# Performance work log

Hardware: AMD Instinct MI355X
Metric: run time of the kernel (lower is better)

The kernel has to match this reference:

```python
import jax, jax.numpy as jnp
import numpy as np

N = 100000   # nodes
E = 1600000  # edges
D = 64       # hidden dim == num_features
L = 3        # num_gc_layers
C = 10       # num_classes
G = 512      # num graphs in batch
BN_EPS = 1e-5


def setup_inputs() -> dict:
    key = jax.random.key(0)
    ks = jax.random.split(key, 12)
    s = 1.0 / np.sqrt(D)
    return {
        "x": jax.random.normal(ks[0], (N, D), dtype=jnp.float32),
        "edge_index": jax.random.randint(ks[1], (2, E), 0, N, dtype=jnp.int64),
        "batch": jnp.sort(jax.random.randint(ks[2], (N,), 0, G, dtype=jnp.int64)),
        # GINConv MLP params (layer 0 input dim == D, so all layers stack)
        "w1": jax.random.normal(ks[3], (L, D, D), dtype=jnp.float32) * s,
        "b1": jnp.zeros((L, D), dtype=jnp.float32),
        "w2": jax.random.normal(ks[4], (L, D, D), dtype=jnp.float32) * s,
        "b2": jnp.zeros((L, D), dtype=jnp.float32),
        # BatchNorm affine params
        "gamma": jnp.ones((L, D), dtype=jnp.float32),
        "beta": jnp.zeros((L, D), dtype=jnp.float32),
        # final MLP
        "lin_w": jax.random.normal(ks[5], (L * D, D), dtype=jnp.float32) / np.sqrt(L * D),
        "lin_b": jnp.zeros((D,), dtype=jnp.float32),
        "fin_w": jax.random.normal(ks[6], (D, C), dtype=jnp.float32) * s,
        "fin_b": jnp.zeros((C,), dtype=jnp.float32),
    }


def reference(x, edge_index, batch, w1, b1, w2, b2, gamma, beta, lin_w, lin_b, fin_w, fin_b):
    src, dst = edge_index[0], edge_index[1]
    pooled = []
    h = x
    for i in range(L):
        # GINConv (eps=0): (1+eps)*h_i + sum_{j->i} h_j, then 2-layer MLP
        agg = h + jax.ops.segment_sum(h[src], dst, num_segments=N)  # [N, D]
        z = jax.nn.relu(agg @ w1[i] + b1[i]) @ w2[i] + b2[i]
        z = jax.nn.relu(z)
        # BatchNorm1d (training-mode batch statistics, biased variance)
        mean = jnp.mean(z, axis=0)
        var = jnp.var(z, axis=0)
        h = (z - mean) * (gamma[i] / jnp.sqrt(var + BN_EPS)) + beta[i]
        # global_add_pool: segment-sum over graph ids
        pooled.append(jax.ops.segment_sum(h, batch, num_segments=G))  # [G, D]
    xp = jnp.concatenate(pooled, axis=1)  # [G, L*D]
    out = jax.nn.relu(xp @ lin_w + lin_b) @ fin_w + fin_b  # [G, C]
    return jax.nn.log_softmax(out, axis=-1)
```

## Files before the change

### kernel.cpp

```cpp
#include <hip/hip_runtime.h>

#define BN_EPS 1e-5f
#define TN 128
#define NPB 256
#define BCAP 8192
#define BH_EPB 8192
#define PT_EPB 4096

typedef __attribute__((ext_vector_type(8))) short bf16x8;
typedef __attribute__((ext_vector_type(4))) float f32x4;

static __device__ __forceinline__ unsigned short f2bf(float f) {
    unsigned u = __float_as_uint(f);
    u += 0x7fff + ((u >> 16) & 1);
    return (unsigned short)(u >> 16);
}
static __device__ __forceinline__ float bf2f(unsigned short s) {
    return __uint_as_float(((unsigned)s) << 16);
}

__global__ __launch_bounds__(256) void xbf_kernel(
    const float* __restrict__ x, unsigned short* __restrict__ xbf, int n4)
{
    const int i = blockIdx.x * 256 + threadIdx.x;
    if (i < n4) {
        const float4 v = reinterpret_cast<const float4*>(x)[i];
        ushort4 o;
        o.x = f2bf(v.x); o.y = f2bf(v.y); o.z = f2bf(v.z); o.w = f2bf(v.w);
        reinterpret_cast<ushort4*>(xbf)[i] = o;
    }
}

__global__ __launch_bounds__(256) void wtbf_kernel(
    const float* __restrict__ w1, const float* __restrict__ w2,
    unsigned short* __restrict__ wtb)
{
    __shared__ float sT[64 * 65];
    const int b = blockIdx.x;
    const int t = threadIdx.x;
    const float* src = ((b & 1) ? w2 : w1) + (size_t)(b >> 1) * 4096;
#pragma unroll
    for (int rr = 0; rr < 4; ++rr) {
        const int i = (rr * 256 + t) * 4;
        const float4 v = *reinterpret_cast<const float4*>(src + i);
        const int k = i >> 6, j = i & 63;
        sT[(j + 0) * 65 + k] = v.x;
        sT[(j + 1) * 65 + k] = v.y;
        sT[(j + 2) * 65 + k] = v.z;
        sT[(j + 3) * 65 + k] = v.w;
    }
    __syncthreads();
    const int j = t >> 2;
    const int kb = (t & 3) * 16;
    unsigned short o[16];
#pragma unroll
    for (int i = 0; i < 16; ++i) o[i] = f2bf(sT[j * 65 + kb + i]);
    uint4* dp = reinterpret_cast<uint4*>(wtb + ((size_t)b * 64 + j) * 64 + kb);
    dp[0] = *reinterpret_cast<const uint4*>(&o[0]);
    dp[1] = *reinterpret_cast<const uint4*>(&o[8]);
}

__global__ __launch_bounds__(256) void bh_kernel(
    const int* __restrict__ dst, int* __restrict__ bucketCnt, int E, int NB)
{
    __shared__ int lh[512];
    const int tid = threadIdx.x;
    for (int i = tid; i < NB; i += 256) lh[i] = 0;
    __syncthreads();
    const int base = blockIdx.x * BH_EPB;
#pragma unroll
    for (int k = 0; k < BH_EPB / 256; ++k) {
        const int e = base + k * 256 + tid;
        if (e < E) atomicAdd(&lh[dst[e] >> 8], 1);
    }
    __syncthreads();
    for (int i = tid; i < NB; i += 256) {
        const int c = lh[i];
        if (c > 0) atomicAdd(&bucketCnt[i], c);
    }
}

__global__ __launch_bounds__(512) void bscan_kernel(
    const int* __restrict__ bucketCnt, int* __restrict__ bucketStart,
    int* __restrict__ bucketCursor, int NB)
{
    __shared__ int ls[512];
    const int t = threadIdx.x;
    const int v = (t < NB) ? bucketCnt[t] : 0;
    ls[t] = v;
    __syncthreads();
    for (int off = 1; off < 512; off <<= 1) {
        const int a = ls[t];
        const int b = (t >= off) ? ls[t - off] : 0;
        __syncthreads();
        ls[t] = a + b;
        __syncthreads();
    }
    const int excl = ls[t] - v;
    if (t < NB) { bucketStart[t] = excl; bucketCursor[t] = excl; }
    if (t == 511) bucketStart[NB] = ls[511];
}

__global__ __launch_bounds__(256) void part_kernel(
    const int* __restrict__ src, const int* __restrict__ dst,
    int* __restrict__ bucketCursor, unsigned* __restrict__ part, int E, int NB)
{
    __shared__ int lh[512];
    __shared__ int lbase[512];
    const int tid = threadIdx.x;
    const int base = blockIdx.x * PT_EPB;
    for (int i = tid; i < NB; i += 256) lh[i] = 0;
    __syncthreads();
#pragma unroll
    for (int k = 0; k < PT_EPB / 256; ++k) {
        const int e = base + k * 256 + tid;
        if (e < E) atomicAdd(&lh[dst[e] >> 8], 1);
    }
    __syncthreads();
    for (int i = tid; i < NB; i += 256) {
        const int c = lh[i];
        lbase[i] = (c > 0) ? atomicAdd(&bucketCursor[i], c) : 0;
        lh[i] = 0;
    }
    __syncthreads();
#pragma unroll
    for (int k = 0; k < PT_EPB / 256; ++k) {
        const int e = base + k * 256 + tid;
        if (e < E) {
            const int d = dst[e];
            const int b = d >> 8;
            const int off = atomicAdd(&lh[b], 1);
            part[lbase[b] + off] = ((unsigned)src[e] << 8) | (unsigned)(d & 255);
        }
    }
}

__global__ __launch_bounds__(256) void bcsr_kernel(
    const unsigned* __restrict__ part, const int* __restrict__ bucketStart,
    int* __restrict__ deg, int* __restrict__ rowstart,
    int* __restrict__ eidx, int nN)
{
    __shared__ unsigned sSrc[BCAP];
    __shared__ int ldeg[256], ls[256], lcur[256];
    const int b = blockIdx.x;
    const int tid = threadIdx.x;
    const int sStart = bucketStart[b];
    const int cnt = bucketStart[b + 1] - sStart;
    const bool ldsok = (cnt <= BCAP);

    ldeg[tid] = 0;
    __syncthreads();
    for (int i = tid; i < cnt; i += 256) {
        const unsigned v = part[sStart + i];
        if (ldsok) sSrc[i] = v;
        atomicAdd(&ldeg[v & 255u], 1);
    }
    __syncthreads();
    const int dv = ldeg[tid];
    ls[tid] = dv;
    __syncthreads();
    for (int off = 1; off < 256; off <<= 1) {
        const int a = ls[tid];
        const int c = (tid >= off) ? ls[tid - off] : 0;
        __syncthreads();
        ls[tid] = a + c;
        __syncthreads();
    }
    const int excl = ls[tid] - dv;
    lcur[tid] = excl;
    const int node = b * NPB + tid;
    if (node < nN) {
        deg[node] = dv;
        rowstart[node] = sStart + excl;
    }
    __syncthreads();
    for (int i = tid; i < cnt; i += 256) {
        const unsigned v = ldsok ? sSrc[i] : part[sStart + i];
        const int dloc = (int)(v & 255u);
        const int p = atomicAdd(&lcur[dloc], 1);
        eidx[sStart + p] = (int)(v >> 8);
    }
}

__global__ __launch_bounds__(256) void cnt_kernel(
    const int* __restrict__ batch, int* __restrict__ cnt, int nN)
{
    const int n = blockIdx.x * 256 + threadIdx.x;
    if (n >= nN) return;
    const int g = batch[n];
    const bool firstb = (n == 0) || (batch[n - 1] != g);
    const bool lastb  = (n == nN - 1) || (batch[n + 1] != g);
    if (lastb)  atomicAdd(&cnt[g], n + 1);
    if (firstb) atomicAdd(&cnt[g], -n);
}

__global__ __launch_bounds__(256) void agg_kernel(
    const unsigned short* __restrict__ z, const float* __restrict__ scsh,
    const int* __restrict__ rowstart, const int* __restrict__ deg,
    const int* __restrict__ eidx, unsigned short* __restrict__ agg, int nN)
{
    const int node = blockIdx.x * 4 + (threadIdx.x >> 6);
    if (node >= nN) return;
    const int lane = threadIdx.x & 63;
    const int q = lane >> 4;
    const int fr = (lane & 15) * 4;
    const int rs = rowstart[node];
    const int d = deg[node];

    float a0 = 0.f, a1 = 0.f, a2 = 0.f, a3 = 0.f;
    if (q == 0) {
        const ushort4 v = *reinterpret_cast<const ushort4*>(z + (size_t)node * 64 + fr);
        a0 = bf2f(v.x); a1 = bf2f(v.y); a2 = bf2f(v.z); a3 = bf2f(v.w);
    }
    for (int i = 0; i < d; i += 16) {
        const int j0 = i + q, j1 = j0 + 4, j2 = j0 + 8, j3 = j0 + 12;
        const int c0 = min(j0, d - 1), c1 = min(j1, d - 1);
        const int c2 = min(j2, d - 1), c3 = min(j3, d - 1);
        const int s0 = eidx[rs + c0], s1 = eidx[rs + c1];
        const int s2 = eidx[rs + c2], s3 = eidx[rs + c3];
        const ushort4 v0 = *reinterpret_cast<const ushort4*>(z + (size_t)s0 * 64 + fr);
        const ushort4 v1 = *reinterpret_cast<const ushort4*>(z + (size_t)s1 * 64 + fr);
        const ushort4 v2 = *reinterpret_cast<const ushort4*>(z + (size_t)s2 * 64 + fr);
        const ushort4 v3 = *reinterpret_cast<const ushort4*>(z + (size_t)s3 * 64 + fr);
        const float w0 = (j0 < d) ? 1.f : 0.f;
        const float w1 = (j1 < d) ? 1.f : 0.f;
        const float w2 = (j2 < d) ? 1.f : 0.f;
        const float w3 = (j3 < d) ? 1.f : 0.f;
        a0 = fmaf(w0, bf2f(v0.x), a0); a1 = fmaf(w0, bf2f(v0.y), a1);
        a2 = fmaf(w0, bf2f(v0.z), a2); a3 = fmaf(w0, bf2f(v0.w), a3);
        a0 = fmaf(w1, bf2f(v1.x), a0); a1 = fmaf(w1, bf2f(v1.y), a1);
        a2 = fmaf(w1, bf2f(v1.z), a2); a3 = fmaf(w1, bf2f(v1.w), a3);
        a0 = fmaf(w2, bf2f(v2.x), a0); a1 = fmaf(w2, bf2f(v2.y), a1);
        a2 = fmaf(w2, bf2f(v2.z), a2); a3 = fmaf(w2, bf2f(v2.w), a3);
        a0 = fmaf(w3, bf2f(v3.x), a0); a1 = fmaf(w3, bf2f(v3.y), a1);
        a2 = fmaf(w3, bf2f(v3.z), a2); a3 = fmaf(w3, bf2f(v3.w), a3);
    }
    a0 += __shfl_xor(a0, 16); a0 += __shfl_xor(a0, 32);
    a1 += __shfl_xor(a1, 16); a1 += __shfl_xor(a1, 32);
    a2 += __shfl_xor(a2, 16); a2 += __shfl_xor(a2, 32);
    a3 += __shfl_xor(a3, 16); a3 += __shfl_xor(a3, 32);
    if (lane < 16) {
        float4 sc = make_float4(1.f, 1.f, 1.f, 1.f);
        float4 sh = make_float4(0.f, 0.f, 0.f, 0.f);
        if (scsh) {
            sc = *reinterpret_cast<const float4*>(scsh + fr);
            sh = *reinterpret_cast<const float4*>(scsh + 64 + fr);
        }
        const float c = (float)(d + 1);
        ushort4 ob;
        ob.x = f2bf(fmaf(a0, sc.x, c * sh.x));
        ob.y = f2bf(fmaf(a1, sc.y, c * sh.y));
        ob.z = f2bf(fmaf(a2, sc.z, c * sh.z));
        ob.w = f2bf(fmaf(a3, sc.w, c * sh.w));
        *reinterpret_cast<ushort4*>(agg + (size_t)node * 64 + fr) = ob;
    }
}

__global__ __launch_bounds__(256) void mlp_kernel(
    const unsigned short* __restrict__ agg, const int* __restrict__ batch,
    const unsigned short* __restrict__ wtb, const float* __restrict__ b1,
    const float* __restrict__ b2,
    unsigned short* __restrict__ zout, float* __restrict__ bnstats,
    float* __restrict__ xpz, int layer, int nN, int storeZ)
{
    __shared__ unsigned short sA[128 * 72];
    __shared__ unsigned short sW[2][64 * 72];
    __shared__ float sB[2][64];
    __shared__ float sSum[64], sSq[64];
    __shared__ float sPool[4 * 64];
    __shared__ int sBatch[128];

    const int tid = threadIdx.x;
    const int n0 = blockIdx.x * TN;

    {
        const int row = tid >> 1;
        const int cg = (tid & 1) * 32;
        const int node = n0 + row;
        uint4 v0 = make_uint4(0, 0, 0, 0), v1 = v0, v2 = v0, v3 = v0;
        if (node < nN) {
            const uint4* g = reinterpret_cast<const uint4*>(agg + (size_t)node * 64 + cg);
            v0 = g[0]; v1 = g[1]; v2 = g[2]; v3 = g[3];
        }
        uint4* dp = reinterpret_cast<uint4*>(&sA[row * 72 + cg]);
        dp[0] = v0; dp[1] = v1; dp[2] = v2; dp[3] = v3;
    }
    {
        const int m = tid >> 7;
        const int j = (tid & 127) >> 1;
        const int cg = (tid & 1) * 32;
        const uint4* g = reinterpret_cast<const uint4*>(
            wtb + (((size_t)layer * 2 + m) * 64 + j) * 64 + cg);
        uint4* dp = reinterpret_cast<uint4*>(&sW[m][j * 72 + cg]);
        dp[0] = g[0]; dp[1] = g[1]; dp[2] = g[2]; dp[3] = g[3];
        if (tid < 64) {
            sB[0][tid] = b1[layer * 64 + tid];
            sB[1][tid] = b2[layer * 64 + tid];
            sSum[tid] = 0.f; sSq[tid] = 0.f;
        }
        if (tid < 128) sBatch[tid] = (n0 + tid < nN) ? batch[n0 + tid] : -1;
        sPool[tid] = 0.f;
    }
    __syncthreads();

    const int w  = tid >> 6;
    const int l  = tid & 63;
    const int lr = l & 15;
    const int hi = l >> 4;

    f32x4 acc[2][4];
#pragma unroll
    for (int rt = 0; rt < 2; ++rt)
#pragma unroll
        for (int ct = 0; ct < 4; ++ct) {
            const float bv = sB[0][ct * 16 + lr];
            acc[rt][ct] = (f32x4){bv, bv, bv, bv};
        }
#pragma unroll
    for (int kb = 0; kb < 2; ++kb) {
        const bf16x8 af0 = *reinterpret_cast<const bf16x8*>(&sA[(w * 32 + lr) * 72 + kb * 32 + hi * 8]);
        const bf16x8 af1 = *reinterpret_cast<const bf16x8*>(&sA[(w * 32 + 16 + lr) * 72 + kb * 32 + hi * 8]);
#pragma unroll
        for (int ct = 0; ct < 4; ++ct) {
            const bf16x8 bfr = *reinterpret_cast<const bf16x8*>(&sW[0][(ct * 16 + lr) * 72 + kb * 32 + hi * 8]);
            acc[0][ct] = __builtin_amdgcn_mfma_f32_16x16x32_bf16(af0, bfr, acc[0][ct], 0, 0, 0);
            acc[1][ct] = __builtin_amdgcn_mfma_f32_16x16x32_bf16(af1, bfr, acc[1][ct], 0, 0, 0);
        }
    }
    __syncthreads();
#pragma unroll
    for (int rt = 0; rt < 2; ++rt)
#pragma unroll
        for (int ct = 0; ct < 4; ++ct)
#pragma unroll
            for (int r = 0; r < 4; ++r)
                sA[(w * 32 + rt * 16 + hi * 4 + r) * 72 + ct * 16 + lr] =
                    f2bf(fmaxf(acc[rt][ct][r], 0.f));
    __syncthreads();

#pragma unroll
    for (int rt = 0; rt < 2; ++rt)
#pragma unroll
        for (int ct = 0; ct < 4; ++ct) {
            const float bv = sB[1][ct * 16 + lr];
            acc[rt][ct] = (f32x4){bv, bv, bv, bv};
        }
#pragma unroll
    for (int kb = 0; kb < 2; ++kb) {
        const bf16x8 af0 = *reinterpret_cast<const bf16x8*>(&sA[(w * 32 + lr) * 72 + kb * 32 + hi * 8]);
        const bf16x8 af1 = *reinterpret_cast<const bf16x8*>(&sA[(w * 32 + 16 + lr) * 72 + kb * 32 + hi * 8]);
#pragma unroll
        for (int ct = 0; ct < 4; ++ct) {
            const bf16x8 bfr = *reinterpret_cast<const bf16x8*>(&sW[1][(ct * 16 + lr) * 72 + kb * 32 + hi * 8]);
            acc[0][ct] = __builtin_amdgcn_mfma_f32_16x16x32_bf16(af0, bfr, acc[0][ct], 0, 0, 0);
            acc[1][ct] = __builtin_amdgcn_mfma_f32_16x16x32_bf16(af1, bfr, acc[1][ct], 0, 0, 0);
        }
    }

    const int gfirst = sBatch[0];
#pragma unroll
    for (int ct = 0; ct < 4; ++ct) {
        const int j = ct * 16 + lr;
        float s = 0.f, qsum = 0.f;
#pragma unroll
        for (int rt = 0; rt < 2; ++rt) {
            int curg = -1;
            float ps = 0.f;
#pragma unroll
            for (int r = 0; r < 4; ++r) {
                const int lrow = w * 32 + rt * 16 + hi * 4 + r;
                const int node = n0 + lrow;
                const float v = fmaxf(acc[rt][ct][r], 0.f);
                if (node < nN) {
                    if (storeZ) zout[(size_t)node * 64 + j] = f2bf(v);
                    s += v; qsum += v * v;
                    const int g = sBatch[lrow];
                    if (g != curg) {
                        if (curg >= 0) {
                            const int lg = curg - gfirst;
                            if (lg < 4) atomicAdd(&sPool[lg * 64 + j], ps);
                            else        atomicAdd(&xpz[(size_t)curg * 64 + j], ps);
                        }
                        curg = g; ps = 0.f;
                    }
                    ps += v;
                }
            }
            if (curg >= 0) {
                const int lg = curg - gfirst;
                if (lg < 4) atomicAdd(&sPool[lg * 64 + j], ps);
                else        atomicAdd(&xpz[(size_t)curg * 64 + j], ps);
            }
        }
        s += __shfl_xor(s, 16); s += __shfl_xor(s, 32);
        qsum += __shfl_xor(qsum, 16); qsum += __shfl_xor(qsum, 32);
        if (hi == 0) { atomicAdd(&sSum[j], s); atomicAdd(&sSq[j], qsum); }
    }
    __syncthreads();
    {
        const int lg = tid >> 6, d = tid & 63;
        const float v = sPool[tid];
        if (v != 0.f) atomicAdd(&xpz[(size_t)(gfirst + lg) * 64 + d], v);
    }
    if (tid < 64) {
        atomicAdd(&bnstats[tid], sSum[tid]);
        atomicAdd(&bnstats[64 + tid], sSq[tid]);
    }
}

__global__ __launch_bounds__(256) void finalize_kernel(
    float* __restrict__ xp, const float* __restrict__ bnstats,
    const float* __restrict__ gamma, const float* __restrict__ beta,
    const int* __restrict__ cnt, float* __restrict__ xpz,
    float* __restrict__ scsh, int layer, int nG, float invN)
{
    const int i = blockIdx.x * 256 + threadIdx.x;
    if (i >= nG * 64) return;
    const int g = i >> 6, d = i & 63;
    const float mean = bnstats[d] * invN;
    const float var  = fmaxf(bnstats[64 + d] * invN - mean * mean, 0.f);
    const float sc = gamma[layer * 64 + d] * rsqrtf(var + BN_EPS);
    const float sh = beta[layer * 64 + d] - mean * sc;
    if (g == 0) { scsh[d] = sc; scsh[64 + d] = sh; }
    xp[(size_t)g * 192 + layer * 64 + d] = fmaf(sc, xpz[i], (float)cnt[g] * sh);
    xpz[i] = 0.f;
}

__global__ __launch_bounds__(256) void final_kernel(
    const float* __restrict__ xp, const float* __restrict__ lin_w,
    const float* __restrict__ lin_b, const float* __restrict__ fin_w,
    const float* __restrict__ fin_b, float* __restrict__ out, int nG)
{
    const int g = (blockIdx.x * 256 + threadIdx.x) >> 6;
    const int lane = threadIdx.x & 63;
    if (g >= nG) return;
    const float* xr = xp + (size_t)g * 192;
    float acc = lin_b[lane];
    for (int k = 0; k < 192; ++k) acc = fmaf(xr[k], lin_w[k * 64 + lane], acc);
    const float t = fmaxf(acc, 0.f);
    float o[10];
#pragma unroll
    for (int c = 0; c < 10; ++c) {
        float p = t * fin_w[lane * 10 + c];
#pragma unroll
        for (int off = 32; off > 0; off >>= 1) p += __shfl_xor(p, off);
        o[c] = p + fin_b[c];
    }
    float m = o[0];
#pragma unroll
    for (int c = 1; c < 10; ++c) m = fmaxf(m, o[c]);
    float Z = 0.f;
#pragma unroll
    for (int c = 0; c < 10; ++c) Z += expf(o[c] - m);
    const float lz = m + logf(Z);
#pragma unroll
    for (int c = 0; c < 10; ++c)
        if (lane == c) out[(size_t)g * 10 + c] = o[c] - lz;
}

extern "C" void kernel_launch(void* const* d_in, const int* in_sizes, int n_in,
                              void* d_out, int out_size, void* d_ws, size_t ws_size,
                              hipStream_t stream)
{
    const float* x     = (const float*)d_in[0];
    const int*   ei    = (const int*)d_in[1];
    const int*   batch = (const int*)d_in[2];
    const float* w1    = (const float*)d_in[3];
    const float* b1    = (const float*)d_in[4];
    const float* w2    = (const float*)d_in[5];
    const float* b2    = (const float*)d_in[6];
    const float* gamma = (const float*)d_in[7];
    const float* beta  = (const float*)d_in[8];
    const float* lin_w = (const float*)d_in[9];
    const float* lin_b = (const float*)d_in[10];
    const float* fin_w = (const float*)d_in[11];
    const float* fin_b = (const float*)d_in[12];
    float* out = (float*)d_out;

    const int N = in_sizes[0] / 64;
    const int E = in_sizes[1] / 2;
    const int L = in_sizes[3] / 4096;
    const int G = out_size / 10;
    const float invN = 1.0f / (float)N;
    const int NB = (N + NPB - 1) / NPB;

    char* ws = (char*)d_ws;
    size_t off = 0;
    auto alloc = [&](size_t bytes) -> void* {
        void* p = ws + off;
        off += (bytes + 255) & ~(size_t)255;
        return p;
    };
    unsigned short* xbf = (unsigned short*)alloc((size_t)N * 64 * 2);
    unsigned short* z0  = (unsigned short*)alloc((size_t)N * 64 * 2);
    unsigned short* z1  = (unsigned short*)alloc((size_t)N * 64 * 2);
    unsigned short* aggbuf = (unsigned short*)alloc((size_t)N * 64 * 2);
    unsigned short* wtb = (unsigned short*)alloc((size_t)L * 2 * 4096 * 2);
    float* xp      = (float*)alloc((size_t)G * 192 * 4);
    float* xpz     = (float*)alloc((size_t)G * 64 * 4);
    float* bnstats = (float*)alloc((size_t)L * 128 * 4);
    float* scsh    = (float*)alloc(128 * 4);
    int*   cnt      = (int*)alloc((size_t)G * 4);
    int*   deg      = (int*)alloc((size_t)N * 4);
    int*   rowstart = (int*)alloc((size_t)N * 4);
    int*   eidx     = (int*)alloc((size_t)E * 4);
    unsigned* part  = (unsigned*)alloc((size_t)E * 4);
    int*   bucketCnt    = (int*)alloc((size_t)NB * 4);
    int*   bucketStart  = (int*)alloc((size_t)(NB + 1) * 4);
    int*   bucketCursor = (int*)alloc((size_t)NB * 4);

    const int* srcIdx = ei;
    const int* dstIdx = ei + E;

    hipMemsetAsync(bucketCnt, 0, (size_t)NB * 4, stream);
    hipMemsetAsync(bnstats, 0, (size_t)L * 128 * 4, stream);
    hipMemsetAsync(xpz, 0, (size_t)G * 64 * 4, stream);
    hipMemsetAsync(cnt, 0, (size_t)G * 4, stream);
    bh_kernel<<<(E + BH_EPB - 1) / BH_EPB, 256, 0, stream>>>(dstIdx, bucketCnt, E, NB);
    bscan_kernel<<<1, 512, 0, stream>>>(bucketCnt, bucketStart, bucketCursor, NB);
    part_kernel<<<(E + PT_EPB - 1) / PT_EPB, 256, 0, stream>>>(
        srcIdx, dstIdx, bucketCursor, part, E, NB);
    bcsr_kernel<<<NB, 256, 0, stream>>>(part, bucketStart, deg, rowstart, eidx, N);
    cnt_kernel<<<(N + 255) / 256, 256, 0, stream>>>(batch, cnt, N);
    xbf_kernel<<<(N * 16 + 255) / 256, 256, 0, stream>>>(x, xbf, N * 16);
    wtbf_kernel<<<L * 2, 256, 0, stream>>>(w1, w2, wtb);

    const int nAggBlk = (N + 3) / 4;
    const int nMlpBlk = (N + TN - 1) / TN;
    unsigned short* zprev = xbf;
    unsigned short* zcur = z0;
    for (int l = 0; l < L; ++l) {
        agg_kernel<<<nAggBlk, 256, 0, stream>>>(
            zprev, (l == 0) ? nullptr : scsh,
            rowstart, deg, eidx, aggbuf, N);
        mlp_kernel<<<nMlpBlk, 256, 0, stream>>>(
            aggbuf, batch, wtb, b1, b2,
            zcur, bnstats + (size_t)l * 128, xpz, l, N, (l < L - 1) ? 1 : 0);
        finalize_kernel<<<(G * 64 + 255) / 256, 256, 0, stream>>>(
            xp, bnstats + (size_t)l * 128, gamma, beta, cnt, xpz, scsh, l, G, invN);
        zprev = zcur;
        zcur = (zcur == z0) ? z1 : z0;
    }
    final_kernel<<<(G * 64 + 255) / 256, 256, 0, stream>>>(xp, lin_w, lin_b,
                                                           fin_w, fin_b, out, G);
}
```

Before: 323.3 us.

## Fold BN finalize into agg and head kernels, merge prep launches and memsets

Removes the per-layer finalize kernel: the BN scale and shift are recomputed from the raw stats inside agg_kernel, and the pooled outputs of every layer are kept in separate per-layer buffers that a single head kernel normalizes before the final MLP. The xbf, cnt and weight-transpose kernels are merged into one prep launch, and the four memsets become one contiguous memset. The goal is to cut kernel launches and the serial dependencies between them, at the price of redundant per-thread BN math in agg_kernel and a larger pooled buffer.

```diff
diff --git a/kernel.cpp b/kernel.cpp
--- a/kernel.cpp
+++ b/kernel.cpp
@@ -19,26 +19,38 @@
     return __uint_as_float(((unsigned)s) << 16);
 }
 
-__global__ __launch_bounds__(256) void xbf_kernel(
-    const float* __restrict__ x, unsigned short* __restrict__ xbf, int n4)
-{
-    const int i = blockIdx.x * 256 + threadIdx.x;
-    if (i < n4) {
-        const float4 v = reinterpret_cast<const float4*>(x)[i];
-        ushort4 o;
-        o.x = f2bf(v.x); o.y = f2bf(v.y); o.z = f2bf(v.z); o.w = f2bf(v.w);
-        reinterpret_cast<ushort4*>(xbf)[i] = o;
-    }
-}
-
-__global__ __launch_bounds__(256) void wtbf_kernel(
+__global__ __launch_bounds__(256) void prep_kernel(
+    const float* __restrict__ x, unsigned short* __restrict__ xbf, int n4, int n4b,
+    const int* __restrict__ batch, int* __restrict__ cnt, int nN, int ncb,
     const float* __restrict__ w1, const float* __restrict__ w2,
     unsigned short* __restrict__ wtb)
 {
     __shared__ float sT[64 * 65];
     const int b = blockIdx.x;
     const int t = threadIdx.x;
-    const float* src = ((b & 1) ? w2 : w1) + (size_t)(b >> 1) * 4096;
+    if (b < n4b) {
+        const int i = b * 256 + t;
+        if (i < n4) {
+            const float4 v = reinterpret_cast<const float4*>(x)[i];
+            ushort4 o;
+            o.x = f2bf(v.x); o.y = f2bf(v.y); o.z = f2bf(v.z); o.w = f2bf(v.w);
+            reinterpret_cast<ushort4*>(xbf)[i] = o;
+        }
+        return;
+    }
+    if (b < n4b + ncb) {
+        const int n = (b - n4b) * 256 + t;
+        if (n < nN) {
+            const int g = batch[n];
+            const bool firstb = (n == 0) || (batch[n - 1] != g);
+            const bool lastb  = (n == nN - 1) || (batch[n + 1] != g);
+            if (lastb)  atomicAdd(&cnt[g], n + 1);
+            if (firstb) atomicAdd(&cnt[g], -n);
+        }
+        return;
+    }
+    const int bw = b - n4b - ncb;
+    const float* src = ((bw & 1) ? w2 : w1) + (size_t)(bw >> 1) * 4096;
 #pragma unroll
     for (int rr = 0; rr < 4; ++rr) {
         const int i = (rr * 256 + t) * 4;
@@ -55,7 +67,7 @@
     unsigned short o[16];
 #pragma unroll
     for (int i = 0; i < 16; ++i) o[i] = f2bf(sT[j * 65 + kb + i]);
-    uint4* dp = reinterpret_cast<uint4*>(wtb + ((size_t)b * 64 + j) * 64 + kb);
+    uint4* dp = reinterpret_cast<uint4*>(wtb + ((size_t)bw * 64 + j) * 64 + kb);
     dp[0] = *reinterpret_cast<const uint4*>(&o[0]);
     dp[1] = *reinterpret_cast<const uint4*>(&o[8]);
 }
@@ -182,22 +194,12 @@
     }
 }
 
-__global__ __launch_bounds__(256) void cnt_kernel(
-    const int* __restrict__ batch, int* __restrict__ cnt, int nN)
-{
-    const int n = blockIdx.x * 256 + threadIdx.x;
-    if (n >= nN) return;
-    const int g = batch[n];
-    const bool firstb = (n == 0) || (batch[n - 1] != g);
-    const bool lastb  = (n == nN - 1) || (batch[n + 1] != g);
-    if (lastb)  atomicAdd(&cnt[g], n + 1);
-    if (firstb) atomicAdd(&cnt[g], -n);
-}
-
 __global__ __launch_bounds__(256) void agg_kernel(
-    const unsigned short* __restrict__ z, const float* __restrict__ scsh,
+    const unsigned short* __restrict__ z, const float* __restrict__ bnprev,
+    const float* __restrict__ gamma, const float* __restrict__ beta,
     const int* __restrict__ rowstart, const int* __restrict__ deg,
-    const int* __restrict__ eidx, unsigned short* __restrict__ agg, int nN)
+    const int* __restrict__ eidx, unsigned short* __restrict__ agg,
+    int layerPrev, int nN, float invN)
 {
     const int node = blockIdx.x * 4 + (threadIdx.x >> 6);
     if (node >= nN) return;
@@ -240,18 +242,23 @@
     a2 += __shfl_xor(a2, 16); a2 += __shfl_xor(a2, 32);
     a3 += __shfl_xor(a3, 16); a3 += __shfl_xor(a3, 32);
     if (lane < 16) {
-        float4 sc = make_float4(1.f, 1.f, 1.f, 1.f);
-        float4 sh = make_float4(0.f, 0.f, 0.f, 0.f);
-        if (scsh) {
-            sc = *reinterpret_cast<const float4*>(scsh + fr);
-            sh = *reinterpret_cast<const float4*>(scsh + 64 + fr);
+        float sc[4] = {1.f, 1.f, 1.f, 1.f};
+        float sh[4] = {0.f, 0.f, 0.f, 0.f};
+        if (bnprev) {
+#pragma unroll
+            for (int k = 0; k < 4; ++k) {
+                const float mean = bnprev[fr + k] * invN;
+                const float var = fmaxf(bnprev[64 + fr + k] * invN - mean * mean, 0.f);
+                sc[k] = gamma[layerPrev * 64 + fr + k] * rsqrtf(var + BN_EPS);
+                sh[k] = beta[layerPrev * 64 + fr + k] - mean * sc[k];
+            }
         }
         const float c = (float)(d + 1);
         ushort4 ob;
-        ob.x = f2bf(fmaf(a0, sc.x, c * sh.x));
-        ob.y = f2bf(fmaf(a1, sc.y, c * sh.y));
-        ob.z = f2bf(fmaf(a2, sc.z, c * sh.z));
-        ob.w = f2bf(fmaf(a3, sc.w, c * sh.w));
+        ob.x = f2bf(fmaf(a0, sc[0], c * sh[0]));
+        ob.y = f2bf(fmaf(a1, sc[1], c * sh[1]));
+        ob.z = f2bf(fmaf(a2, sc[2], c * sh[2]));
+        ob.w = f2bf(fmaf(a3, sc[3], c * sh[3]));
         *reinterpret_cast<ushort4*>(agg + (size_t)node * 64 + fr) = ob;
     }
 }
@@ -408,34 +415,33 @@
     }
 }
 
-__global__ __launch_bounds__(256) void finalize_kernel(
-    float* __restrict__ xp, const float* __restrict__ bnstats,
+__global__ __launch_bounds__(256) void head_kernel(
+    const float* __restrict__ xpz, const float* __restrict__ bnstats,
     const float* __restrict__ gamma, const float* __restrict__ beta,
-    const int* __restrict__ cnt, float* __restrict__ xpz,
-    float* __restrict__ scsh, int layer, int nG, float invN)
-{
-    const int i = blockIdx.x * 256 + threadIdx.x;
-    if (i >= nG * 64) return;
-    const int g = i >> 6, d = i & 63;
-    const float mean = bnstats[d] * invN;
-    const float var  = fmaxf(bnstats[64 + d] * invN - mean * mean, 0.f);
-    const float sc = gamma[layer * 64 + d] * rsqrtf(var + BN_EPS);
-    const float sh = beta[layer * 64 + d] - mean * sc;
-    if (g == 0) { scsh[d] = sc; scsh[64 + d] = sh; }
-    xp[(size_t)g * 192 + layer * 64 + d] = fmaf(sc, xpz[i], (float)cnt[g] * sh);
-    xpz[i] = 0.f;
-}
-
-__global__ __launch_bounds__(256) void final_kernel(
-    const float* __restrict__ xp, const float* __restrict__ lin_w,
-    const float* __restrict__ lin_b, const float* __restrict__ fin_w,
-    const float* __restrict__ fin_b, float* __restrict__ out, int nG)
-{
-    const int g = (blockIdx.x * 256 + threadIdx.x) >> 6;
+    const int* __restrict__ cnt,
+    const float* __restrict__ lin_w, const float* __restrict__ lin_b,
+    const float* __restrict__ fin_w, const float* __restrict__ fin_b,
+    float* __restrict__ out, int nG, int nL, float invN)
+{
+    __shared__ float sX[4][192];
+    const int wv = threadIdx.x >> 6;
     const int lane = threadIdx.x & 63;
-    if (g >= nG) return;
-    const float* xr = xp + (size_t)g * 192;
+    const int g = blockIdx.x * 4 + wv;
+    const bool act = (g < nG);
+    const float cg = act ? (float)cnt[g] : 0.f;
+    const size_t G64 = (size_t)nG * 64;
+    for (int ll = 0; ll < nL; ++ll) {
+        const float mean = bnstats[ll * 128 + lane] * invN;
+        const float var  = fmaxf(bnstats[ll * 128 + 64 + lane] * invN - mean * mean, 0.f);
+        const float sc = gamma[ll * 64 + lane] * rsqrtf(var + BN_EPS);
+        const float sh = beta[ll * 64 + lane] - mean * sc;
+        const float pv = act ? xpz[ll * G64 + (size_t)g * 64 + lane] : 0.f;
+        sX[wv][ll * 64 + lane] = fmaf(sc, pv, cg * sh);
+    }
+    __syncthreads();
+    if (!act) return;
     float acc = lin_b[lane];
+    const float* xr = sX[wv];
     for (int k = 0; k < 192; ++k) acc = fmaf(xr[k], lin_w[k * 64 + lane], acc);
     const float t = fmaxf(acc, 0.f);
     float o[10];
@@ -496,34 +502,36 @@
     unsigned short* z1  = (unsigned short*)alloc((size_t)N * 64 * 2);
     unsigned short* aggbuf = (unsigned short*)alloc((size_t)N * 64 * 2);
     unsigned short* wtb = (unsigned short*)alloc((size_t)L * 2 * 4096 * 2);
-    float* xp      = (float*)alloc((size_t)G * 192 * 4);
-    float* xpz     = (float*)alloc((size_t)G * 64 * 4);
-    float* bnstats = (float*)alloc((size_t)L * 128 * 4);
-    float* scsh    = (float*)alloc(128 * 4);
-    int*   cnt      = (int*)alloc((size_t)G * 4);
     int*   deg      = (int*)alloc((size_t)N * 4);
     int*   rowstart = (int*)alloc((size_t)N * 4);
     int*   eidx     = (int*)alloc((size_t)E * 4);
     unsigned* part  = (unsigned*)alloc((size_t)E * 4);
-    int*   bucketCnt    = (int*)alloc((size_t)NB * 4);
     int*   bucketStart  = (int*)alloc((size_t)(NB + 1) * 4);
     int*   bucketCursor = (int*)alloc((size_t)NB * 4);
+    const size_t zeroOff = off;
+    int*   bucketCnt = (int*)alloc((size_t)NB * 4);
+    int*   cnt       = (int*)alloc((size_t)G * 4);
+    float* bnstats   = (float*)alloc((size_t)L * 128 * 4);
+    float* xpz       = (float*)alloc((size_t)L * G * 64 * 4);
+    const size_t zeroBytes = off - zeroOff;
 
     const int* srcIdx = ei;
     const int* dstIdx = ei + E;
 
-    hipMemsetAsync(bucketCnt, 0, (size_t)NB * 4, stream);
-    hipMemsetAsync(bnstats, 0, (size_t)L * 128 * 4, stream);
-    hipMemsetAsync(xpz, 0, (size_t)G * 64 * 4, stream);
-    hipMemsetAsync(cnt, 0, (size_t)G * 4, stream);
+    hipMemsetAsync(ws + zeroOff, 0, zeroBytes, stream);
+
     bh_kernel<<<(E + BH_EPB - 1) / BH_EPB, 256, 0, stream>>>(dstIdx, bucketCnt, E, NB);
     bscan_kernel<<<1, 512, 0, stream>>>(bucketCnt, bucketStart, bucketCursor, NB);
     part_kernel<<<(E + PT_EPB - 1) / PT_EPB, 256, 0, stream>>>(
         srcIdx, dstIdx, bucketCursor, part, E, NB);
     bcsr_kernel<<<NB, 256, 0, stream>>>(part, bucketStart, deg, rowstart, eidx, N);
-    cnt_kernel<<<(N + 255) / 256, 256, 0, stream>>>(batch, cnt, N);
-    xbf_kernel<<<(N * 16 + 255) / 256, 256, 0, stream>>>(x, xbf, N * 16);
-    wtbf_kernel<<<L * 2, 256, 0, stream>>>(w1, w2, wtb);
+    {
+        const int n4 = N * 16;
+        const int n4b = (n4 + 255) / 256;
+        const int ncb = (N + 255) / 256;
+        prep_kernel<<<n4b + ncb + L * 2, 256, 0, stream>>>(
+            x, xbf, n4, n4b, batch, cnt, N, ncb, w1, w2, wtb);
+    }
 
     const int nAggBlk = (N + 3) / 4;
     const int nMlpBlk = (N + TN - 1) / TN;
@@ -531,16 +539,16 @@
     unsigned short* zcur = z0;
     for (int l = 0; l < L; ++l) {
         agg_kernel<<<nAggBlk, 256, 0, stream>>>(
-            zprev, (l == 0) ? nullptr : scsh,
-            rowstart, deg, eidx, aggbuf, N);
+            zprev, (l == 0) ? nullptr : (bnstats + (size_t)(l - 1) * 128),
+            gamma, beta, rowstart, deg, eidx, aggbuf, l - 1, N, invN);
         mlp_kernel<<<nMlpBlk, 256, 0, stream>>>(
             aggbuf, batch, wtb, b1, b2,
-            zcur, bnstats + (size_t)l * 128, xpz, l, N, (l < L - 1) ? 1 : 0);
-        finalize_kernel<<<(G * 64 + 255) / 256, 256, 0, stream>>>(
-            xp, bnstats + (size_t)l * 128, gamma, beta, cnt, xpz, scsh, l, G, invN);
+            zcur, bnstats + (size_t)l * 128, xpz + (size_t)l * G * 64,
+            l, N, (l < L - 1) ? 1 : 0);
         zprev = zcur;
         zcur = (zcur == z0) ? z1 : z0;
     }
-    final_kernel<<<(G * 64 + 255) / 256, 256, 0, stream>>>(xp, lin_w, lin_b,
-                                                           fin_w, fin_b, out, G);
-}
+    head_kernel<<<(G + 3) / 4, 256, 0, stream>>>(
+        xpz, bnstats, gamma, beta, cnt, lin_w, lin_b, fin_w, fin_b,
+        out, G, L, invN);
+}
```

New measurement: 316.0 us. -2.3%, faster.
